# Kernel optimization log

Hardware: AMD Instinct MI355X
Metric: run time of the kernel (lower is better)

## Reference

```python
import jax, jax.numpy as jnp
import numpy as np
import math

H = 128
W = 128
CAM_DIST = 2.0
FOVY = 1.57 / 2.0
SIGMAINV = 7000.0
ERODE = 7
PAD = (ERODE - 1) // 2


def quat_to_rotmat(q):
    # q: [B,4] WXYZ (kornia convention), normalized first
    q = q / jnp.linalg.norm(q, axis=-1, keepdims=True)
    w, x, y, z = q[..., 0], q[..., 1], q[..., 2], q[..., 3]
    R = jnp.stack([
        1 - 2 * (y * y + z * z), 2 * (x * y - w * z), 2 * (x * z + w * y),
        2 * (x * y + w * z), 1 - 2 * (x * x + z * z), 2 * (y * z - w * x),
        2 * (x * z - w * y), 2 * (y * z + w * x), 1 - 2 * (x * x + y * y),
    ], axis=-1)
    return R.reshape(q.shape[:-1] + (3, 3))


def _edge(ax, ay, bx, by, px, py):
    return (px - ax) * (by - ay) - (py - ay) * (bx - ax)


def rasterize(fv_img, fz, fnz, ffeat):
    # fv_img [F,3,2] image-space verts, fz [F,3] camera-space z, fnz [F] normal z, ffeat [F,3,C]
    xs = (jnp.arange(W) + 0.5) / W * 2.0 - 1.0
    ys = 1.0 - (jnp.arange(H) + 0.5) / H * 2.0
    gx, gy = jnp.meshgrid(xs, ys, indexing='xy')   # [H,W]
    PX = gx.reshape(-1, 1)                          # [P,1]
    PY = gy.reshape(-1, 1)
    ax, ay = fv_img[:, 0, 0], fv_img[:, 0, 1]
    bx, by = fv_img[:, 1, 0], fv_img[:, 1, 1]
    cx, cy = fv_img[:, 2, 0], fv_img[:, 2, 1]
    area = _edge(ax, ay, bx, by, cx, cy)            # [F]
    area_s = jnp.where(jnp.abs(area) < 1e-10, 1e-10, area)
    w0 = _edge(bx, by, cx, cy, PX, PY) / area_s     # [P,F] barycentric
    w1 = _edge(cx, cy, ax, ay, PX, PY) / area_s
    w2 = _edge(ax, ay, bx, by, PX, PY) / area_s
    inside = (w0 >= 0) & (w1 >= 0) & (w2 >= 0) & (jnp.abs(area) > 1e-10)
    zpix = w0 * fz[:, 0] + w1 * fz[:, 1] + w2 * fz[:, 2]
    valid = inside & (fnz > 0)                      # back-face cull
    score = jnp.where(valid, zpix, -1e30)           # camera looks down -z: max z is closest
    best = jnp.argmax(score, axis=1)                # [P]
    has = jnp.any(valid, axis=1)
    red = jnp.where(has, best, -1)
    P = PX.shape[0]
    pidx = jnp.arange(P)
    wsel = jnp.stack([w0[pidx, best], w1[pidx, best], w2[pidx, best]], -1)  # [P,3]
    feat = jnp.einsum('pk,pkc->pc', wsel, ffeat[best])
    feat = jnp.where(has[:, None], feat, 0.0)
    # DIB-R soft silhouette: p_f = exp(-d^2*sigmainv) (d=0 inside), A = 1 - prod(1-p_f)
    def seg_d2(a, b):
        abx, aby = b[:, 0] - a[:, 0], b[:, 1] - a[:, 1]
        apx, apy = PX - a[:, 0], PY - a[:, 1]
        t = jnp.clip((apx * abx + apy * aby) / (abx * abx + aby * aby + 1e-12), 0.0, 1.0)
        dx, dy = apx - t * abx, apy - t * aby
        return dx * dx + dy * dy
    d2 = jnp.minimum(jnp.minimum(seg_d2(fv_img[:, 0], fv_img[:, 1]),
                                 seg_d2(fv_img[:, 1], fv_img[:, 2])),
                     seg_d2(fv_img[:, 2], fv_img[:, 0]))
    d2 = jnp.where(inside, 0.0, d2)
    prob = jnp.clip(jnp.exp(-d2 * SIGMAINV), 0.0, 1.0 - 1e-4) * (fnz > 0)
    soft = 1.0 - jnp.exp(jnp.sum(jnp.log1p(-prob), axis=1))
    C = ffeat.shape[-1]
    return feat.reshape(H, W, C), soft.reshape(H, W), red.reshape(H, W)


def bilinear(tex, uv):
    # tex [3,T,T], uv [H,W,2] in [0,1]; torch grid_sample-style bilinear, align_corners=False
    T = tex.shape[-1]
    u = jnp.clip(uv[..., 0], 0.0, 1.0)
    v = jnp.clip(uv[..., 1], 0.0, 1.0)
    x = u * T - 0.5
    y = (1.0 - v) * T - 0.5   # kaolin texture_mapping flips v
    x0 = jnp.floor(x)
    y0 = jnp.floor(y)
    wx = x - x0
    wy = y - y0
    x0i = jnp.clip(x0.astype(jnp.int32), 0, T - 1)
    x1i = jnp.clip(x0i + 1, 0, T - 1)
    y0i = jnp.clip(y0.astype(jnp.int32), 0, T - 1)
    y1i = jnp.clip(y0i + 1, 0, T - 1)
    t00 = tex[:, y0i, x0i]
    t01 = tex[:, y0i, x1i]
    t10 = tex[:, y1i, x0i]
    t11 = tex[:, y1i, x1i]
    return (1 - wy) * ((1 - wx) * t00 + wx * t01) + wy * ((1 - wx) * t10 + wx * t11)


def render_frame(tvec, q, unit_vertices, faces, face_features, texture_maps):
    R = quat_to_rotmat(q)                                        # [B,3,3]
    verts = jnp.einsum('bij,bvj->bvi', R, unit_vertices) + tvec  # rotate about origin + translate
    p_cam = verts - jnp.array([0.0, 0.0, CAM_DIST], dtype=verts.dtype)  # camera at (0,0,d), look-at origin
    ratio = W / H
    tanf = math.tan(FOVY / 2.0)
    negz = -p_cam[..., 2]
    img = jnp.stack([p_cam[..., 0] / (ratio * tanf) / negz,
                     p_cam[..., 1] / tanf / negz], axis=-1)      # [B,V,2]
    fv_img = img[:, faces]                                       # [B,F,3,2]
    fz = p_cam[..., 2][:, faces]                                 # [B,F,3]
    fv_cam = p_cam[:, faces]                                     # [B,F,3,3]
    n = jnp.cross(fv_cam[:, :, 1] - fv_cam[:, :, 0], fv_cam[:, :, 2] - fv_cam[:, :, 0])
    fnz = n[..., 2] / (jnp.linalg.norm(n, axis=-1) + 1e-10)      # [B,F]
    feat, soft, red = jax.vmap(rasterize)(fv_img, fz, fnz, face_features)
    rgb = jax.vmap(bilinear)(texture_maps, feat)                 # [B,3,H,W]
    # erosion with all-ones kernel == grayscale min-pool (borders padded with +inf)
    mask = jax.lax.reduce_window(soft, jnp.inf, jax.lax.min,
                                 (1, ERODE, ERODE), (1, 1, 1),
                                 [(0, 0), (PAD, PAD), (PAD, PAD)])
    Fn = faces.shape[0]
    redw = jnp.where(red < 0, Fn - 1, red)                       # torch -1 index wraps to last face
    depth = jax.vmap(lambda z, r: z[r].mean(-1))(fz, redw)       # [B,H,W]
    return jnp.concatenate([rgb, mask[:, None], depth[:, None]], axis=1)  # [B,5,H,W]


def setup_inputs():
    key = jax.random.key(0)
    ks = jax.random.split(key, 6)
    B, NF, V, F, T = 1, 4, 256, 512, 256
    return {
        'translation': jax.random.uniform(ks[0], (B, 1, NF, 3), minval=-0.3, maxval=0.3),
        'quaternion': jax.random.normal(ks[1], (B, NF, 4)),
        'unit_vertices': jax.random.uniform(ks[2], (B, V, 3), minval=-0.5, maxval=0.5),
        'face_features': jax.random.uniform(ks[3], (B, F, 3, 2)),
        'texture_maps': jax.random.uniform(ks[4], (B, 3, T, T)),
        'faces': jax.random.randint(ks[5], (F, 3), 0, V),
    }


def reference(translation, quaternion, unit_vertices, face_features, texture_maps, faces):
    tseq = jnp.moveaxis(translation, 2, 0)   # [NF,B,1,3]
    qseq = jnp.moveaxis(quaternion, 1, 0)    # [NF,B,4]
    def step(carry, tq):
        t, q = tq
        return carry, render_frame(t, q, unit_vertices, faces, face_features, texture_maps)
    _, outs = jax.lax.scan(step, None, (tseq, qseq))  # [NF,B,5,H,W]
    return jnp.moveaxis(outs, 0, 1)[:, :, None]       # [B,NF,1,5,H,W]
```

## Files before the change

### kernel.cpp

```cpp
#include <hip/hip_runtime.h>
#include <math.h>

#define NFRM 4
#define NFACE 512
#define TT 256
#define REC 32
#define TANF32 0.413980342966f
#define LOG1M_CONST -9.21017456f
#define D2_CUTOFF 0.004286f
#define MARGIN 0.0656f

__device__ __forceinline__ float fm(float a, float b) { return __fmul_rn(a, b); }
__device__ __forceinline__ float fa2(float a, float b) { return __fadd_rn(a, b); }
__device__ __forceinline__ float fs2(float a, float b) { return __fsub_rn(a, b); }
__device__ __forceinline__ float fd2(float a, float b) { return __fdiv_rn(a, b); }


__global__ void setup_kernel(const float* __restrict__ trans,
                             const float* __restrict__ quat,
                             const float* __restrict__ uverts,
                             const int* __restrict__ faces,
                             float* __restrict__ recs,
                             float4* __restrict__ bbox4) {
    int idx = blockIdx.x * blockDim.x + threadIdx.x;
    if (idx >= NFRM * NFACE) return;
    int frame = idx >> 9;
    int face  = idx & (NFACE - 1);

    float qw = quat[frame * 4 + 0];
    float qx = quat[frame * 4 + 1];
    float qy = quat[frame * 4 + 2];
    float qz = quat[frame * 4 + 3];
    float qn = sqrtf(fa2(fa2(fa2(fm(qw, qw), fm(qx, qx)), fm(qy, qy)), fm(qz, qz)));
    qw = fd2(qw, qn); qx = fd2(qx, qn); qy = fd2(qy, qn); qz = fd2(qz, qn);

    float r00 = fs2(1.f, fm(2.f, fa2(fm(qy, qy), fm(qz, qz))));
    float r01 = fm(2.f, fs2(fm(qx, qy), fm(qw, qz)));
    float r02 = fm(2.f, fa2(fm(qx, qz), fm(qw, qy)));
    float r10 = fm(2.f, fa2(fm(qx, qy), fm(qw, qz)));
    float r11 = fs2(1.f, fm(2.f, fa2(fm(qx, qx), fm(qz, qz))));
    float r12 = fm(2.f, fs2(fm(qy, qz), fm(qw, qx)));
    float r20 = fm(2.f, fs2(fm(qx, qz), fm(qw, qy)));
    float r21 = fm(2.f, fa2(fm(qy, qz), fm(qw, qx)));
    float r22 = fs2(1.f, fm(2.f, fa2(fm(qx, qx), fm(qy, qy))));

    float tx = trans[frame * 3 + 0];
    float ty = trans[frame * 3 + 1];
    float tz = trans[frame * 3 + 2];

    float camx[3], camy[3], camz[3], ix[3], iy[3];
    for (int k = 0; k < 3; ++k) {
        int vi = faces[face * 3 + k];
        float ux = uverts[vi * 3 + 0];
        float uy = uverts[vi * 3 + 1];
        float uz = uverts[vi * 3 + 2];
        float X = fa2(fa2(fa2(fm(r00, ux), fm(r01, uy)), fm(r02, uz)), tx);
        float Y = fa2(fa2(fa2(fm(r10, ux), fm(r11, uy)), fm(r12, uz)), ty);
        float Z = fs2(fa2(fa2(fa2(fm(r20, ux), fm(r21, uy)), fm(r22, uz)), tz), 2.0f);
        float negz = -Z;
        camx[k] = X; camy[k] = Y; camz[k] = Z;
        ix[k] = fd2(fd2(X, TANF32), negz);
        iy[k] = fd2(fd2(Y, TANF32), negz);
    }

    float e1cx = fs2(camx[1], camx[0]), e1cy = fs2(camy[1], camy[0]);
    float e2cx = fs2(camx[2], camx[0]), e2cy = fs2(camy[2], camy[0]);
    float nz = fs2(fm(e1cx, e2cy), fm(e1cy, e2cx));

    float ax = ix[0], ay = iy[0], bx = ix[1], by = iy[1], cx = ix[2], cy = iy[2];
    float area = fs2(fm(fs2(cx, ax), fs2(by, ay)), fm(fs2(cy, ay), fs2(bx, ax)));
    bool areaok = fabsf(area) > 1e-10f;
    float area_s = (fabsf(area) < 1e-10f) ? 1e-10f : area;

    float e0x = fs2(cx, bx), e0y = fs2(cy, by);
    float e1x = fs2(ax, cx), e1y = fs2(ay, cy);
    float e2x = fs2(bx, ax), e2y = fs2(by, ay);

    float* r = recs + (size_t)idx * REC;
    r[0] = 0.f; r[1] = 0.f; r[2] = 0.f; r[3] = 0.f;
    r[4] = areaok ? 1.f : 2.f;
    r[5] = (area_s >= 0.f) ? 1.f : -1.f;
    r[6] = fd2(1.0f, area_s);
    r[7] = 0.f;
    r[8]  = ax; r[9]  = ay; r[10] = e2x; r[11] = e2y;
    r[12] = bx; r[13] = by; r[14] = e0x; r[15] = e0y;
    r[16] = cx; r[17] = cy; r[18] = e1x; r[19] = e1y;
    r[20] = camz[0]; r[21] = camz[1]; r[22] = camz[2]; r[23] = 0.f;
    r[24] = fd2(1.0f, fa2(fa2(fm(e2x, e2x), fm(e2y, e2y)), 1e-12f));
    r[25] = fd2(1.0f, fa2(fa2(fm(e0x, e0x), fm(e0y, e0y)), 1e-12f));
    r[26] = fd2(1.0f, fa2(fa2(fm(e1x, e1x), fm(e1y, e1y)), 1e-12f));
    r[27] = 0.f; r[28] = 0.f; r[29] = 0.f; r[30] = 0.f; r[31] = 0.f;

    float4 bb;
    if (nz > 0.f) {
        bb.x = fminf(fminf(ax, bx), cx);
        bb.y = fmaxf(fmaxf(ax, bx), cx);
        bb.z = fminf(fminf(ay, by), cy);
        bb.w = fmaxf(fmaxf(ay, by), cy);
    } else {
        bb.x = 1e30f; bb.y = -1e30f; bb.z = 1e30f; bb.w = -1e30f;
    }
    bbox4[idx] = bb;
}

__global__ __launch_bounds__(256, 4) void raster_kernel(
        const float* __restrict__ recs,
        const float4* __restrict__ bbox4,
        const float* __restrict__ ffeat,
        const float* __restrict__ tex,
        float* __restrict__ out,
        float* __restrict__ softbuf) {
    __shared__ int s_list[NFACE];
    __shared__ int s_cnt[4];
    __shared__ float s_score[256], s_w0[256], s_w1[256], s_w2[256], s_acc[256];
    __shared__ int s_best[256];

    int frame   = blockIdx.x >> 8;
    int tileIdx = blockIdx.x & 255;
    int txo = (tileIdx & 15) * 8;
    int tyo = (tileIdx >> 4) * 8;

    int chunk = threadIdx.x >> 6;
    int lane  = threadIdx.x & 63;
    int w = txo + (lane & 7);
    int h = tyo + (lane >> 3);
    int p = h * 128 + w;
    float px = (w + 0.5f) * (1.0f / 64.0f) - 1.0f;
    float py = 1.0f - (h + 0.5f) * (1.0f / 64.0f);

    float txmin = (txo + 0.5f) * (1.0f / 64.0f) - 1.0f - MARGIN;
    float txmax = (txo + 7.5f) * (1.0f / 64.0f) - 1.0f + MARGIN;
    float tymin = 1.0f - (tyo + 7.5f) * (1.0f / 64.0f) - MARGIN;
    float tymax = 1.0f - (tyo + 0.5f) * (1.0f / 64.0f) + MARGIN;

    const float4* bbF = bbox4 + frame * NFACE;
    unsigned long long m0, m1;
    {
        float4 b0 = bbF[chunk * 128 + lane];
        float4 b1 = bbF[chunk * 128 + 64 + lane];
        bool p0 = (b0.x <= txmax) & (b0.y >= txmin) & (b0.z <= tymax) & (b0.w >= tymin);
        bool p1 = (b1.x <= txmax) & (b1.y >= txmin) & (b1.z <= tymax) & (b1.w >= tymin);
        m0 = __ballot(p0);
        m1 = __ballot(p1);
    }
    if (lane == 0) s_cnt[chunk] = __popcll(m0) + __popcll(m1);
    __syncthreads();
    int base = 0;
    for (int c = 0; c < chunk; ++c) base += s_cnt[c];
    int total = s_cnt[0] + s_cnt[1] + s_cnt[2] + s_cnt[3];
    unsigned long long ltmask = (1ull << lane) - 1ull;
    if ((m0 >> lane) & 1)
        s_list[base + __popcll(m0 & ltmask)] = chunk * 128 + lane;
    if ((m1 >> lane) & 1)
        s_list[base + __popcll(m0) + __popcll(m1 & ltmask)] = chunk * 128 + 64 + lane;
    __syncthreads();

    const float* recF = recs + (size_t)frame * NFACE * REC;
    float bestScore = -1e30f;
    int best = -1;
    float bw0 = 0.f, bw1 = 0.f, bw2 = 0.f;
    float acc = 0.f;

    int lo = (total * chunk) >> 2;
    int hi = (total * (chunk + 1)) >> 2;
    #pragma unroll 2
    for (int i = lo; i < hi; ++i) {
        int f = __builtin_amdgcn_readfirstlane(s_list[i]);
        const float* r = recF + ((size_t)f << 5);
        float flag = r[4];
        float ax = r[8],  ay = r[9],  e2x = r[10], e2y = r[11];
        float bx = r[12], by = r[13], e0x = r[14], e0y = r[15];
        float cx = r[16], cy = r[17], e1x = r[18], e1y = r[19];
        float apx = fs2(px, ax), apy = fs2(py, ay);
        float bpx = fs2(px, bx), bpy = fs2(py, by);
        float cpx = fs2(px, cx), cpy = fs2(py, cy);
        float n0 = fs2(fm(bpx, e0y), fm(bpy, e0x));
        float n1 = fs2(fm(cpx, e1y), fm(cpy, e1x));
        float n2 = fs2(fm(apx, e2y), fm(apy, e2x));
        float sgn = r[5];
        bool inside = (flag == 1.f) & (fm(n0, sgn) >= 0.f)
                    & (fm(n1, sgn) >= 0.f) & (fm(n2, sgn) >= 0.f);
        if (inside) {
            float ia = r[6];
            float w0 = fm(n0, ia), w1v = fm(n1, ia), w2v = fm(n2, ia);
            float zpix = fa2(fa2(fm(w0, r[20]), fm(w1v, r[21])), fm(w2v, r[22]));
            if (zpix > bestScore) {
                bestScore = zpix; best = f; bw0 = w0; bw1 = w1v; bw2 = w2v;
            }
            acc += LOG1M_CONST;
        } else {
            float t0 = fminf(fmaxf((apx * e2x + apy * e2y) * r[24], 0.f), 1.f);
            float dx0 = apx - t0 * e2x, dy0 = apy - t0 * e2y;
            float d2 = dx0 * dx0 + dy0 * dy0;
            float t1 = fminf(fmaxf((bpx * e0x + bpy * e0y) * r[25], 0.f), 1.f);
            float dx1 = bpx - t1 * e0x, dy1 = bpy - t1 * e0y;
            d2 = fminf(d2, dx1 * dx1 + dy1 * dy1);
            float t2 = fminf(fmaxf((cpx * e1x + cpy * e1y) * r[26], 0.f), 1.f);
            float dx2 = cpx - t2 * e1x, dy2 = cpy - t2 * e1y;
            d2 = fminf(d2, dx2 * dx2 + dy2 * dy2);
            if (d2 < D2_CUTOFF) {
                float pr = fminf(__expf(d2 * -7000.f), 0.9999f);
                acc += __logf(1.0f - pr);
            }
        }
    }

    s_score[threadIdx.x] = bestScore;
    s_best[threadIdx.x] = best;
    s_w0[threadIdx.x] = bw0; s_w1[threadIdx.x] = bw1; s_w2[threadIdx.x] = bw2;
    s_acc[threadIdx.x] = acc;
    __syncthreads();

    if (threadIdx.x < 64) {
        int i = threadIdx.x;
        bestScore = s_score[i]; best = s_best[i];
        bw0 = s_w0[i]; bw1 = s_w1[i]; bw2 = s_w2[i];
        acc = s_acc[i];
        for (int c = 1; c < 4; ++c) {
            int j = c * 64 + i;
            float sc = s_score[j];
            if (sc > bestScore) {
                bestScore = sc; best = s_best[j];
                bw0 = s_w0[j]; bw1 = s_w1[j]; bw2 = s_w2[j];
            }
            acc += s_acc[j];
        }
        float fu = 0.f, fv = 0.f;
        if (best >= 0) {
            const float* fb = ffeat + best * 6;
            fu = bw0 * fb[0] + bw1 * fb[2] + bw2 * fb[4];
            fv = bw0 * fb[1] + bw1 * fb[3] + bw2 * fb[5];
        }
        float u = fminf(fmaxf(fu, 0.f), 1.f);
        float v = fminf(fmaxf(fv, 0.f), 1.f);
        float x = u * (float)TT - 0.5f;
        float y = (1.0f - v) * (float)TT - 0.5f;
        float x0f = floorf(x), y0f = floorf(y);
        float wx = x - x0f, wy = y - y0f;
        int x0 = min(max((int)x0f, 0), TT - 1);
        int x1 = min(x0 + 1, TT - 1);
        int y0 = min(max((int)y0f, 0), TT - 1);
        int y1 = min(y0 + 1, TT - 1);
        size_t obase = (size_t)frame * 5 * 16384 + p;
        for (int c = 0; c < 3; ++c) {
            const float* tc = tex + c * (TT * TT);
            float t00 = tc[y0 * TT + x0];
            float t01 = tc[y0 * TT + x1];
            float t10 = tc[y1 * TT + x0];
            float t11 = tc[y1 * TT + x1];
            float rgb = (1.f - wy) * ((1.f - wx) * t00 + wx * t01)
                      + wy * ((1.f - wx) * t10 + wx * t11);
            out[obase + (size_t)c * 16384] = rgb;
        }
        int redw = (best >= 0) ? best : (NFACE - 1);
        const float* rr = recF + ((size_t)redw << 5);
        float depth = fd2(fa2(fa2(rr[20], rr[21]), rr[22]), 3.0f);
        out[obase + 4ull * 16384] = depth;
        float soft = 1.0f - __expf(acc);
        softbuf[frame * 16384 + p] = soft;
    }
}

__global__ void minpool_kernel(const float* __restrict__ softbuf,
                               float* __restrict__ out) {
    int idx = blockIdx.x * 256 + threadIdx.x;
    if (idx >= NFRM * 16384) return;
    int frame = idx >> 14;
    int p = idx & 16383;
    int h = p >> 7, w = p & 127;
    const float* sb = softbuf + frame * 16384;
    float m = INFINITY;
    int h0 = max(h - 3, 0), h1 = min(h + 3, 127);
    int w0 = max(w - 3, 0), w1 = min(w + 3, 127);
    for (int hh = h0; hh <= h1; ++hh)
        for (int ww = w0; ww <= w1; ++ww)
            m = fminf(m, sb[hh * 128 + ww]);
    out[(size_t)frame * 5 * 16384 + 3ull * 16384 + p] = m;
}

extern "C" void kernel_launch(void* const* d_in, const int* in_sizes, int n_in,
                              void* d_out, int out_size, void* d_ws, size_t ws_size,
                              hipStream_t stream) {
    const float* trans  = (const float*)d_in[0];
    const float* quat   = (const float*)d_in[1];
    const float* uverts = (const float*)d_in[2];
    const float* ffeat  = (const float*)d_in[3];
    const float* tex    = (const float*)d_in[4];
    const int*   faces  = (const int*)d_in[5];
    float* out = (float*)d_out;

    float* recs    = (float*)d_ws;
    float4* bbox4  = (float4*)(recs + NFRM * NFACE * REC);
    float* softbuf = (float*)(bbox4 + NFRM * NFACE);

    setup_kernel<<<(NFRM * NFACE + 255) / 256, 256, 0, stream>>>(trans, quat, uverts, faces, recs, bbox4);
    raster_kernel<<<NFRM * 256, 256, 0, stream>>>(recs, bbox4, ffeat, tex, out, softbuf);
    minpool_kernel<<<NFRM * 16384 / 256, 256, 0, stream>>>(softbuf, out);
}
```

Measured before the change: 95.85 us.

## Split faces across two raster blocks per tile and merge in combine kernel

The raster kernel now splits the 512 faces into two halves, launching twice as many blocks, each writing partial depth-test and soft-silhouette results to workspace. A new combine kernel merges the two halves, then does texture sampling, depth and soft-mask output. Tile order is bit-reversed to spread work across CUs, and face indices are loaded once per 64-face batch and broadcast with readlane instead of one LDS read per face. This adds a kernel launch and extra global traffic for the partial buffers in exchange for more parallelism and better load balance. Tie-breaking between halves uses a strict greater-than comparison, so the lower-index face wins ties, which matches argmax.

```diff
diff --git a/kernel.cpp b/kernel.cpp
--- a/kernel.cpp
+++ b/kernel.cpp
@@ -3,6 +3,7 @@
 
 #define NFRM 4
 #define NFACE 512
+#define HALF 256
 #define TT 256
 #define REC 32
 #define TANF32 0.413980342966f
@@ -106,17 +107,19 @@
 __global__ __launch_bounds__(256, 4) void raster_kernel(
         const float* __restrict__ recs,
         const float4* __restrict__ bbox4,
-        const float* __restrict__ ffeat,
-        const float* __restrict__ tex,
-        float* __restrict__ out,
-        float* __restrict__ softbuf) {
-    __shared__ int s_list[NFACE];
+        float* __restrict__ pscore, int* __restrict__ pbest,
+        float* __restrict__ pw0, float* __restrict__ pw1,
+        float* __restrict__ pw2, float* __restrict__ pacc) {
+    __shared__ int s_list[HALF];
     __shared__ int s_cnt[4];
     __shared__ float s_score[256], s_w0[256], s_w1[256], s_w2[256], s_acc[256];
     __shared__ int s_best[256];
 
-    int frame   = blockIdx.x >> 8;
-    int tileIdx = blockIdx.x & 255;
+    int b = blockIdx.x;
+    int tileIdx = (int)(__brev((unsigned)(b & 255)) >> 24);
+    int frame = (b >> 8) & 3;
+    int half  = b >> 10;
+    int fbase = half * HALF;
     int txo = (tileIdx & 15) * 8;
     int tyo = (tileIdx >> 4) * 8;
 
@@ -133,27 +136,20 @@
     float tymin = 1.0f - (tyo + 7.5f) * (1.0f / 64.0f) - MARGIN;
     float tymax = 1.0f - (tyo + 0.5f) * (1.0f / 64.0f) + MARGIN;
 
-    const float4* bbF = bbox4 + frame * NFACE;
-    unsigned long long m0, m1;
     {
-        float4 b0 = bbF[chunk * 128 + lane];
-        float4 b1 = bbF[chunk * 128 + 64 + lane];
-        bool p0 = (b0.x <= txmax) & (b0.y >= txmin) & (b0.z <= tymax) & (b0.w >= tymin);
-        bool p1 = (b1.x <= txmax) & (b1.y >= txmin) & (b1.z <= tymax) & (b1.w >= tymin);
-        m0 = __ballot(p0);
-        m1 = __ballot(p1);
-    }
-    if (lane == 0) s_cnt[chunk] = __popcll(m0) + __popcll(m1);
-    __syncthreads();
-    int base = 0;
-    for (int c = 0; c < chunk; ++c) base += s_cnt[c];
+        int face = fbase + chunk * 64 + lane;
+        float4 bb = bbox4[frame * NFACE + face];
+        bool hit = (bb.x <= txmax) & (bb.y >= txmin) & (bb.z <= tymax) & (bb.w >= tymin);
+        unsigned long long m = __ballot(hit);
+        if (lane == 0) s_cnt[chunk] = __popcll(m);
+        __syncthreads();
+        int base = 0;
+        for (int c = 0; c < chunk; ++c) base += s_cnt[c];
+        unsigned long long ltmask = (1ull << lane) - 1ull;
+        if (hit) s_list[base + __popcll(m & ltmask)] = face;
+        __syncthreads();
+    }
     int total = s_cnt[0] + s_cnt[1] + s_cnt[2] + s_cnt[3];
-    unsigned long long ltmask = (1ull << lane) - 1ull;
-    if ((m0 >> lane) & 1)
-        s_list[base + __popcll(m0 & ltmask)] = chunk * 128 + lane;
-    if ((m1 >> lane) & 1)
-        s_list[base + __popcll(m0) + __popcll(m1 & ltmask)] = chunk * 128 + 64 + lane;
-    __syncthreads();
 
     const float* recF = recs + (size_t)frame * NFACE * REC;
     float bestScore = -1e30f;
@@ -163,44 +159,49 @@
 
     int lo = (total * chunk) >> 2;
     int hi = (total * (chunk + 1)) >> 2;
-    #pragma unroll 2
-    for (int i = lo; i < hi; ++i) {
-        int f = __builtin_amdgcn_readfirstlane(s_list[i]);
-        const float* r = recF + ((size_t)f << 5);
-        float flag = r[4];
-        float ax = r[8],  ay = r[9],  e2x = r[10], e2y = r[11];
-        float bx = r[12], by = r[13], e0x = r[14], e0y = r[15];
-        float cx = r[16], cy = r[17], e1x = r[18], e1y = r[19];
-        float apx = fs2(px, ax), apy = fs2(py, ay);
-        float bpx = fs2(px, bx), bpy = fs2(py, by);
-        float cpx = fs2(px, cx), cpy = fs2(py, cy);
-        float n0 = fs2(fm(bpx, e0y), fm(bpy, e0x));
-        float n1 = fs2(fm(cpx, e1y), fm(cpy, e1x));
-        float n2 = fs2(fm(apx, e2y), fm(apy, e2x));
-        float sgn = r[5];
-        bool inside = (flag == 1.f) & (fm(n0, sgn) >= 0.f)
-                    & (fm(n1, sgn) >= 0.f) & (fm(n2, sgn) >= 0.f);
-        if (inside) {
-            float ia = r[6];
-            float w0 = fm(n0, ia), w1v = fm(n1, ia), w2v = fm(n2, ia);
-            float zpix = fa2(fa2(fm(w0, r[20]), fm(w1v, r[21])), fm(w2v, r[22]));
-            if (zpix > bestScore) {
-                bestScore = zpix; best = f; bw0 = w0; bw1 = w1v; bw2 = w2v;
-            }
-            acc += LOG1M_CONST;
-        } else {
-            float t0 = fminf(fmaxf((apx * e2x + apy * e2y) * r[24], 0.f), 1.f);
-            float dx0 = apx - t0 * e2x, dy0 = apy - t0 * e2y;
-            float d2 = dx0 * dx0 + dy0 * dy0;
-            float t1 = fminf(fmaxf((bpx * e0x + bpy * e0y) * r[25], 0.f), 1.f);
-            float dx1 = bpx - t1 * e0x, dy1 = bpy - t1 * e0y;
-            d2 = fminf(d2, dx1 * dx1 + dy1 * dy1);
-            float t2 = fminf(fmaxf((cpx * e1x + cpy * e1y) * r[26], 0.f), 1.f);
-            float dx2 = cpx - t2 * e1x, dy2 = cpy - t2 * e1y;
-            d2 = fminf(d2, dx2 * dx2 + dy2 * dy2);
-            if (d2 < D2_CUTOFF) {
-                float pr = fminf(__expf(d2 * -7000.f), 0.9999f);
-                acc += __logf(1.0f - pr);
+    for (int base = lo; base < hi; base += 64) {
+        int nb = min(64, hi - base);
+        int li = base + ((lane < nb) ? lane : (nb - 1));
+        int vlist = s_list[li];
+        #pragma unroll 2
+        for (int j = 0; j < nb; ++j) {
+            int f = __builtin_amdgcn_readlane(vlist, j);
+            const float* r = recF + ((size_t)f << 5);
+            float flag = r[4];
+            float ax = r[8],  ay = r[9],  e2x = r[10], e2y = r[11];
+            float bx = r[12], by = r[13], e0x = r[14], e0y = r[15];
+            float cx = r[16], cy = r[17], e1x = r[18], e1y = r[19];
+            float apx = fs2(px, ax), apy = fs2(py, ay);
+            float bpx = fs2(px, bx), bpy = fs2(py, by);
+            float cpx = fs2(px, cx), cpy = fs2(py, cy);
+            float n0 = fs2(fm(bpx, e0y), fm(bpy, e0x));
+            float n1 = fs2(fm(cpx, e1y), fm(cpy, e1x));
+            float n2 = fs2(fm(apx, e2y), fm(apy, e2x));
+            float sgn = r[5];
+            bool inside = (flag == 1.f) & (fm(n0, sgn) >= 0.f)
+                        & (fm(n1, sgn) >= 0.f) & (fm(n2, sgn) >= 0.f);
+            if (inside) {
+                float ia = r[6];
+                float w0 = fm(n0, ia), w1v = fm(n1, ia), w2v = fm(n2, ia);
+                float zpix = fa2(fa2(fm(w0, r[20]), fm(w1v, r[21])), fm(w2v, r[22]));
+                if (zpix > bestScore) {
+                    bestScore = zpix; best = f; bw0 = w0; bw1 = w1v; bw2 = w2v;
+                }
+                acc += LOG1M_CONST;
+            } else {
+                float t0 = fminf(fmaxf((apx * e2x + apy * e2y) * r[24], 0.f), 1.f);
+                float dx0 = apx - t0 * e2x, dy0 = apy - t0 * e2y;
+                float d2 = dx0 * dx0 + dy0 * dy0;
+                float t1 = fminf(fmaxf((bpx * e0x + bpy * e0y) * r[25], 0.f), 1.f);
+                float dx1 = bpx - t1 * e0x, dy1 = bpy - t1 * e0y;
+                d2 = fminf(d2, dx1 * dx1 + dy1 * dy1);
+                float t2 = fminf(fmaxf((cpx * e1x + cpy * e1y) * r[26], 0.f), 1.f);
+                float dx2 = cpx - t2 * e1x, dy2 = cpy - t2 * e1y;
+                d2 = fminf(d2, dx2 * dx2 + dy2 * dy2);
+                if (d2 < D2_CUTOFF) {
+                    float pr = fminf(__expf(d2 * -7000.f), 0.9999f);
+                    acc += __logf(1.0f - pr);
+                }
             }
         }
     }
@@ -225,40 +226,69 @@
             }
             acc += s_acc[j];
         }
-        float fu = 0.f, fv = 0.f;
-        if (best >= 0) {
-            const float* fb = ffeat + best * 6;
-            fu = bw0 * fb[0] + bw1 * fb[2] + bw2 * fb[4];
-            fv = bw0 * fb[1] + bw1 * fb[3] + bw2 * fb[5];
-        }
-        float u = fminf(fmaxf(fu, 0.f), 1.f);
-        float v = fminf(fmaxf(fv, 0.f), 1.f);
-        float x = u * (float)TT - 0.5f;
-        float y = (1.0f - v) * (float)TT - 0.5f;
-        float x0f = floorf(x), y0f = floorf(y);
-        float wx = x - x0f, wy = y - y0f;
-        int x0 = min(max((int)x0f, 0), TT - 1);
-        int x1 = min(x0 + 1, TT - 1);
-        int y0 = min(max((int)y0f, 0), TT - 1);
-        int y1 = min(y0 + 1, TT - 1);
-        size_t obase = (size_t)frame * 5 * 16384 + p;
-        for (int c = 0; c < 3; ++c) {
-            const float* tc = tex + c * (TT * TT);
-            float t00 = tc[y0 * TT + x0];
-            float t01 = tc[y0 * TT + x1];
-            float t10 = tc[y1 * TT + x0];
-            float t11 = tc[y1 * TT + x1];
-            float rgb = (1.f - wy) * ((1.f - wx) * t00 + wx * t01)
-                      + wy * ((1.f - wx) * t10 + wx * t11);
-            out[obase + (size_t)c * 16384] = rgb;
-        }
-        int redw = (best >= 0) ? best : (NFACE - 1);
-        const float* rr = recF + ((size_t)redw << 5);
-        float depth = fd2(fa2(fa2(rr[20], rr[21]), rr[22]), 3.0f);
-        out[obase + 4ull * 16384] = depth;
-        float soft = 1.0f - __expf(acc);
-        softbuf[frame * 16384 + p] = soft;
-    }
+        size_t o = ((size_t)half * NFRM + frame) * 16384 + p;
+        pscore[o] = bestScore; pbest[o] = best;
+        pw0[o] = bw0; pw1[o] = bw1; pw2[o] = bw2; pacc[o] = acc;
+    }
+}
+
+__global__ void combine_kernel(
+        const float* __restrict__ pscore, const int* __restrict__ pbest,
+        const float* __restrict__ pw0, const float* __restrict__ pw1,
+        const float* __restrict__ pw2, const float* __restrict__ pacc,
+        const float* __restrict__ recs,
+        const float* __restrict__ ffeat,
+        const float* __restrict__ tex,
+        float* __restrict__ out,
+        float* __restrict__ softbuf) {
+    int idx = blockIdx.x * 256 + threadIdx.x;
+    if (idx >= NFRM * 16384) return;
+    int frame = idx >> 14;
+    int p = idx & 16383;
+    size_t o0 = (size_t)frame * 16384 + p;
+    size_t o1 = o0 + (size_t)NFRM * 16384;
+
+    float s0 = pscore[o0], s1 = pscore[o1];
+    bool take1 = (s1 > s0);
+    int best   = take1 ? pbest[o1] : pbest[o0];
+    float bw0  = take1 ? pw0[o1] : pw0[o0];
+    float bw1  = take1 ? pw1[o1] : pw1[o0];
+    float bw2  = take1 ? pw2[o1] : pw2[o0];
+    float acc  = pacc[o0] + pacc[o1];
+
+    float fu = 0.f, fv = 0.f;
+    if (best >= 0) {
+        const float* fb = ffeat + best * 6;
+        fu = bw0 * fb[0] + bw1 * fb[2] + bw2 * fb[4];
+        fv = bw0 * fb[1] + bw1 * fb[3] + bw2 * fb[5];
+    }
+    float u = fminf(fmaxf(fu, 0.f), 1.f);
+    float v = fminf(fmaxf(fv, 0.f), 1.f);
+    float x = u * (float)TT - 0.5f;
+    float y = (1.0f - v) * (float)TT - 0.5f;
+    float x0f = floorf(x), y0f = floorf(y);
+    float wx = x - x0f, wy = y - y0f;
+    int x0 = min(max((int)x0f, 0), TT - 1);
+    int x1 = min(x0 + 1, TT - 1);
+    int y0 = min(max((int)y0f, 0), TT - 1);
+    int y1 = min(y0 + 1, TT - 1);
+    size_t obase = (size_t)frame * 5 * 16384 + p;
+    for (int c = 0; c < 3; ++c) {
+        const float* tc = tex + c * (TT * TT);
+        float t00 = tc[y0 * TT + x0];
+        float t01 = tc[y0 * TT + x1];
+        float t10 = tc[y1 * TT + x0];
+        float t11 = tc[y1 * TT + x1];
+        float rgb = (1.f - wy) * ((1.f - wx) * t00 + wx * t01)
+                  + wy * ((1.f - wx) * t10 + wx * t11);
+        out[obase + (size_t)c * 16384] = rgb;
+    }
+    int redw = (best >= 0) ? best : (NFACE - 1);
+    const float* rr = recs + (size_t)frame * NFACE * REC + ((size_t)redw << 5);
+    float depth = fd2(fa2(fa2(rr[20], rr[21]), rr[22]), 3.0f);
+    out[obase + 4ull * 16384] = depth;
+    float soft = 1.0f - __expf(acc);
+    softbuf[(size_t)frame * 16384 + p] = soft;
 }
 
 __global__ void minpool_kernel(const float* __restrict__ softbuf,
@@ -289,11 +319,22 @@
     const int*   faces  = (const int*)d_in[5];
     float* out = (float*)d_out;
 
+    const size_t NPIX = (size_t)NFRM * 16384;
     float* recs    = (float*)d_ws;
     float4* bbox4  = (float4*)(recs + NFRM * NFACE * REC);
-    float* softbuf = (float*)(bbox4 + NFRM * NFACE);
-
-    setup_kernel<<<(NFRM * NFACE + 255) / 256, 256, 0, stream>>>(trans, quat, uverts, faces, recs, bbox4);
-    raster_kernel<<<NFRM * 256, 256, 0, stream>>>(recs, bbox4, ffeat, tex, out, softbuf);
-    minpool_kernel<<<NFRM * 16384 / 256, 256, 0, stream>>>(softbuf, out);
-}
+    float* pscore  = (float*)(bbox4 + NFRM * NFACE);
+    int*   pbest   = (int*)(pscore + 2 * NPIX);
+    float* pw0     = (float*)(pbest + 2 * NPIX);
+    float* pw1     = pw0 + 2 * NPIX;
+    float* pw2     = pw1 + 2 * NPIX;
+    float* pacc    = pw2 + 2 * NPIX;
+    float* softbuf = pacc + 2 * NPIX;
+
+    setup_kernel<<<(NFRM * NFACE + 255) / 256, 256, 0, stream>>>(
+        trans, quat, uverts, faces, recs, bbox4);
+    raster_kernel<<<NFRM * 256 * 2, 256, 0, stream>>>(
+        recs, bbox4, pscore, pbest, pw0, pw1, pw2, pacc);
+    combine_kernel<<<(NFRM * 16384) / 256, 256, 0, stream>>>(
+        pscore, pbest, pw0, pw1, pw2, pacc, recs, ffeat, tex, out, softbuf);
+    minpool_kernel<<<(NFRM * 16384) / 256, 256, 0, stream>>>(softbuf, out);
+}
```

Measured after the change: 96.57 us. No clear change (+0.8%).

## Prefetch next face record, bit-reverse tile order, and pack edge math

Applied to the files above, without the earlier changes.

The per-face loop now loads the next face's record while the current one is evaluated, a software double-buffer meant to hide the scalar load latency. Tile indices are bit-reversed so neighbouring blocks map to spatially scattered tiles, aiming to even out per-workgroup load across CUs. The outside-triangle distance math is written with 2-wide vectors so the compiler can emit packed FP32 ops. Prefetching raises register pressure under the launch bound, and the packed ops may change rounding slightly in the soft-silhouette path.

```diff
diff --git a/kernel.cpp b/kernel.cpp
--- a/kernel.cpp
+++ b/kernel.cpp
@@ -9,6 +9,8 @@
 #define LOG1M_CONST -9.21017456f
 #define D2_CUTOFF 0.004286f
 #define MARGIN 0.0656f
+
+typedef float v2f __attribute__((ext_vector_type(2)));
 
 __device__ __forceinline__ float fm(float a, float b) { return __fmul_rn(a, b); }
 __device__ __forceinline__ float fa2(float a, float b) { return __fadd_rn(a, b); }
@@ -103,6 +105,23 @@
     bbox4[idx] = bb;
 }
 
+struct FRec {
+    float flag, sgn, ia;
+    float ax, ay, e2x, e2y, bx, by, e0x, e0y, cx, cy, e1x, e1y;
+    float z0, z1, z2, iL2, iL0, iL1;
+};
+__device__ __forceinline__ FRec loadRec(const float* __restrict__ recF, int f) {
+    const float* r = recF + ((size_t)f << 5);
+    FRec o;
+    o.flag = r[4];  o.sgn = r[5];  o.ia  = r[6];
+    o.ax = r[8];  o.ay = r[9];  o.e2x = r[10]; o.e2y = r[11];
+    o.bx = r[12]; o.by = r[13]; o.e0x = r[14]; o.e0y = r[15];
+    o.cx = r[16]; o.cy = r[17]; o.e1x = r[18]; o.e1y = r[19];
+    o.z0 = r[20]; o.z1 = r[21]; o.z2 = r[22];
+    o.iL2 = r[24]; o.iL0 = r[25]; o.iL1 = r[26];
+    return o;
+}
+
 __global__ __launch_bounds__(256, 4) void raster_kernel(
         const float* __restrict__ recs,
         const float4* __restrict__ bbox4,
@@ -115,8 +134,9 @@
     __shared__ float s_score[256], s_w0[256], s_w1[256], s_w2[256], s_acc[256];
     __shared__ int s_best[256];
 
-    int frame   = blockIdx.x >> 8;
-    int tileIdx = blockIdx.x & 255;
+    int b = blockIdx.x;
+    int tileIdx = (int)(__brev((unsigned)(b & 255)) >> 24);
+    int frame = b >> 8;
     int txo = (tileIdx & 15) * 8;
     int tyo = (tileIdx >> 4) * 8;
 
@@ -134,26 +154,23 @@
     float tymax = 1.0f - (tyo + 0.5f) * (1.0f / 64.0f) + MARGIN;
 
     const float4* bbF = bbox4 + frame * NFACE;
-    unsigned long long m0, m1;
     {
         float4 b0 = bbF[chunk * 128 + lane];
         float4 b1 = bbF[chunk * 128 + 64 + lane];
         bool p0 = (b0.x <= txmax) & (b0.y >= txmin) & (b0.z <= tymax) & (b0.w >= tymin);
         bool p1 = (b1.x <= txmax) & (b1.y >= txmin) & (b1.z <= tymax) & (b1.w >= tymin);
-        m0 = __ballot(p0);
-        m1 = __ballot(p1);
-    }
-    if (lane == 0) s_cnt[chunk] = __popcll(m0) + __popcll(m1);
-    __syncthreads();
-    int base = 0;
-    for (int c = 0; c < chunk; ++c) base += s_cnt[c];
+        unsigned long long m0 = __ballot(p0);
+        unsigned long long m1 = __ballot(p1);
+        if (lane == 0) s_cnt[chunk] = __popcll(m0) + __popcll(m1);
+        __syncthreads();
+        int base = 0;
+        for (int c = 0; c < chunk; ++c) base += s_cnt[c];
+        unsigned long long ltmask = (1ull << lane) - 1ull;
+        if (p0) s_list[base + __popcll(m0 & ltmask)] = chunk * 128 + lane;
+        if (p1) s_list[base + __popcll(m0) + __popcll(m1 & ltmask)] = chunk * 128 + 64 + lane;
+        __syncthreads();
+    }
     int total = s_cnt[0] + s_cnt[1] + s_cnt[2] + s_cnt[3];
-    unsigned long long ltmask = (1ull << lane) - 1ull;
-    if ((m0 >> lane) & 1)
-        s_list[base + __popcll(m0 & ltmask)] = chunk * 128 + lane;
-    if ((m1 >> lane) & 1)
-        s_list[base + __popcll(m0) + __popcll(m1 & ltmask)] = chunk * 128 + 64 + lane;
-    __syncthreads();
 
     const float* recF = recs + (size_t)frame * NFACE * REC;
     float bestScore = -1e30f;
@@ -163,45 +180,51 @@
 
     int lo = (total * chunk) >> 2;
     int hi = (total * (chunk + 1)) >> 2;
-    #pragma unroll 2
-    for (int i = lo; i < hi; ++i) {
-        int f = __builtin_amdgcn_readfirstlane(s_list[i]);
-        const float* r = recF + ((size_t)f << 5);
-        float flag = r[4];
-        float ax = r[8],  ay = r[9],  e2x = r[10], e2y = r[11];
-        float bx = r[12], by = r[13], e0x = r[14], e0y = r[15];
-        float cx = r[16], cy = r[17], e1x = r[18], e1y = r[19];
-        float apx = fs2(px, ax), apy = fs2(py, ay);
-        float bpx = fs2(px, bx), bpy = fs2(py, by);
-        float cpx = fs2(px, cx), cpy = fs2(py, cy);
-        float n0 = fs2(fm(bpx, e0y), fm(bpy, e0x));
-        float n1 = fs2(fm(cpx, e1y), fm(cpy, e1x));
-        float n2 = fs2(fm(apx, e2y), fm(apy, e2x));
-        float sgn = r[5];
-        bool inside = (flag == 1.f) & (fm(n0, sgn) >= 0.f)
-                    & (fm(n1, sgn) >= 0.f) & (fm(n2, sgn) >= 0.f);
-        if (inside) {
-            float ia = r[6];
-            float w0 = fm(n0, ia), w1v = fm(n1, ia), w2v = fm(n2, ia);
-            float zpix = fa2(fa2(fm(w0, r[20]), fm(w1v, r[21])), fm(w2v, r[22]));
-            if (zpix > bestScore) {
-                bestScore = zpix; best = f; bw0 = w0; bw1 = w1v; bw2 = w2v;
+    if (lo < hi) {
+        int f_cur = __builtin_amdgcn_readfirstlane(s_list[lo]);
+        FRec cur = loadRec(recF, f_cur);
+        for (int i = lo; i < hi; ++i) {
+            int nj = (i + 1 < hi) ? (i + 1) : i;
+            int f_nxt = __builtin_amdgcn_readfirstlane(s_list[nj]);
+            FRec nxt = loadRec(recF, f_nxt);
+
+            float apx = fs2(px, cur.ax), apy = fs2(py, cur.ay);
+            float bpx = fs2(px, cur.bx), bpy = fs2(py, cur.by);
+            float cpx = fs2(px, cur.cx), cpy = fs2(py, cur.cy);
+            float n0 = fs2(fm(bpx, cur.e0y), fm(bpy, cur.e0x));
+            float n1 = fs2(fm(cpx, cur.e1y), fm(cpy, cur.e1x));
+            float n2 = fs2(fm(apx, cur.e2y), fm(apy, cur.e2x));
+            float sgn = cur.sgn;
+            bool inside = (cur.flag == 1.f) & (fm(n0, sgn) >= 0.f)
+                        & (fm(n1, sgn) >= 0.f) & (fm(n2, sgn) >= 0.f);
+            if (inside) {
+                float ia = cur.ia;
+                float w0 = fm(n0, ia), w1v = fm(n1, ia), w2v = fm(n2, ia);
+                float zpix = fa2(fa2(fm(w0, cur.z0), fm(w1v, cur.z1)), fm(w2v, cur.z2));
+                if (zpix > bestScore) {
+                    bestScore = zpix; best = f_cur; bw0 = w0; bw1 = w1v; bw2 = w2v;
+                }
+                acc += LOG1M_CONST;
+            } else {
+                v2f ap = {apx, apy}, bp = {bpx, bpy}, cp = {cpx, cpy};
+                v2f e2 = {cur.e2x, cur.e2y};
+                v2f e0 = {cur.e0x, cur.e0y};
+                v2f e1 = {cur.e1x, cur.e1y};
+                v2f pa = ap * e2, pb = bp * e0, pc = cp * e1;
+                float t0 = fminf(fmaxf((pa.x + pa.y) * cur.iL2, 0.f), 1.f);
+                float t1 = fminf(fmaxf((pb.x + pb.y) * cur.iL0, 0.f), 1.f);
+                float t2 = fminf(fmaxf((pc.x + pc.y) * cur.iL1, 0.f), 1.f);
+                v2f d0 = ap - t0 * e2;
+                v2f d1 = bp - t1 * e0;
+                v2f d2v = cp - t2 * e1;
+                v2f q0 = d0 * d0, q1 = d1 * d1, q2 = d2v * d2v;
+                float d2 = fminf(fminf(q0.x + q0.y, q1.x + q1.y), q2.x + q2.y);
+                if (d2 < D2_CUTOFF) {
+                    float pr = fminf(__expf(d2 * -7000.f), 0.9999f);
+                    acc += __logf(1.0f - pr);
+                }
             }
-            acc += LOG1M_CONST;
-        } else {
-            float t0 = fminf(fmaxf((apx * e2x + apy * e2y) * r[24], 0.f), 1.f);
-            float dx0 = apx - t0 * e2x, dy0 = apy - t0 * e2y;
-            float d2 = dx0 * dx0 + dy0 * dy0;
-            float t1 = fminf(fmaxf((bpx * e0x + bpy * e0y) * r[25], 0.f), 1.f);
-            float dx1 = bpx - t1 * e0x, dy1 = bpy - t1 * e0y;
-            d2 = fminf(d2, dx1 * dx1 + dy1 * dy1);
-            float t2 = fminf(fmaxf((cpx * e1x + cpy * e1y) * r[26], 0.f), 1.f);
-            float dx2 = cpx - t2 * e1x, dy2 = cpy - t2 * e1y;
-            d2 = fminf(d2, dx2 * dx2 + dy2 * dy2);
-            if (d2 < D2_CUTOFF) {
-                float pr = fminf(__expf(d2 * -7000.f), 0.9999f);
-                acc += __logf(1.0f - pr);
-            }
+            cur = nxt; f_cur = f_nxt;
         }
     }
 
@@ -293,7 +316,9 @@
     float4* bbox4  = (float4*)(recs + NFRM * NFACE * REC);
     float* softbuf = (float*)(bbox4 + NFRM * NFACE);
 
-    setup_kernel<<<(NFRM * NFACE + 255) / 256, 256, 0, stream>>>(trans, quat, uverts, faces, recs, bbox4);
-    raster_kernel<<<NFRM * 256, 256, 0, stream>>>(recs, bbox4, ffeat, tex, out, softbuf);
-    minpool_kernel<<<NFRM * 16384 / 256, 256, 0, stream>>>(softbuf, out);
-}
+    setup_kernel<<<(NFRM * NFACE + 255) / 256, 256, 0, stream>>>(
+        trans, quat, uverts, faces, recs, bbox4);
+    raster_kernel<<<NFRM * 256, 256, 0, stream>>>(
+        recs, bbox4, ffeat, tex, out, softbuf);
+    minpool_kernel<<<(NFRM * 16384) / 256, 256, 0, stream>>>(softbuf, out);
+}
```

Result: no change. 97.15 us (+1.4%).

## Add per-tile edge-distance culling pass and bit-reverse tile ordering

Applied to the files above, without the earlier changes.

Adds a second culling stage after the bounding-box test. For each surviving face it evaluates each edge function at the tile corner most favourable to that edge, and rejects the face when the squared distance to the edge exceeds the soft-silhouette margin. This shrinks the per-pixel face loop, at the cost of an extra compaction pass with two more block barriers per round and a second shared list. Tile indices are also bit-reversed so heavy and light tiles spread across CUs, and the unroll pragma on the main loop is removed.

```diff
diff --git a/kernel.cpp b/kernel.cpp
--- a/kernel.cpp
+++ b/kernel.cpp
@@ -9,6 +9,7 @@
 #define LOG1M_CONST -9.21017456f
 #define D2_CUTOFF 0.004286f
 #define MARGIN 0.0656f
+#define MARGIN2 0.00430336f
 
 __device__ __forceinline__ float fm(float a, float b) { return __fmul_rn(a, b); }
 __device__ __forceinline__ float fa2(float a, float b) { return __fadd_rn(a, b); }
@@ -110,13 +111,15 @@
         const float* __restrict__ tex,
         float* __restrict__ out,
         float* __restrict__ softbuf) {
-    __shared__ int s_list[NFACE];
+    __shared__ int s_listA[NFACE];
+    __shared__ int s_listB[NFACE];
     __shared__ int s_cnt[4];
     __shared__ float s_score[256], s_w0[256], s_w1[256], s_w2[256], s_acc[256];
     __shared__ int s_best[256];
 
-    int frame   = blockIdx.x >> 8;
-    int tileIdx = blockIdx.x & 255;
+    int b = blockIdx.x;
+    int tileIdx = (int)(__brev((unsigned)(b & 255)) >> 24);
+    int frame = b >> 8;
     int txo = (tileIdx & 15) * 8;
     int tyo = (tileIdx >> 4) * 8;
 
@@ -128,44 +131,81 @@
     float px = (w + 0.5f) * (1.0f / 64.0f) - 1.0f;
     float py = 1.0f - (h + 0.5f) * (1.0f / 64.0f);
 
-    float txmin = (txo + 0.5f) * (1.0f / 64.0f) - 1.0f - MARGIN;
-    float txmax = (txo + 7.5f) * (1.0f / 64.0f) - 1.0f + MARGIN;
-    float tymin = 1.0f - (tyo + 7.5f) * (1.0f / 64.0f) - MARGIN;
-    float tymax = 1.0f - (tyo + 0.5f) * (1.0f / 64.0f) + MARGIN;
-
-    const float4* bbF = bbox4 + frame * NFACE;
-    unsigned long long m0, m1;
+    float X0 = (txo + 0.5f) * (1.0f / 64.0f) - 1.0f;
+    float X1 = (txo + 7.5f) * (1.0f / 64.0f) - 1.0f;
+    float Y0 = 1.0f - (tyo + 7.5f) * (1.0f / 64.0f);
+    float Y1 = 1.0f - (tyo + 0.5f) * (1.0f / 64.0f);
+    float txmin = X0 - MARGIN, txmax = X1 + MARGIN;
+    float tymin = Y0 - MARGIN, tymax = Y1 + MARGIN;
+
+    const float* recF = recs + (size_t)frame * NFACE * REC;
+    unsigned long long ltmask = (1ull << lane) - 1ull;
+
+    int totalA;
     {
+        const float4* bbF = bbox4 + frame * NFACE;
         float4 b0 = bbF[chunk * 128 + lane];
         float4 b1 = bbF[chunk * 128 + 64 + lane];
         bool p0 = (b0.x <= txmax) & (b0.y >= txmin) & (b0.z <= tymax) & (b0.w >= tymin);
         bool p1 = (b1.x <= txmax) & (b1.y >= txmin) & (b1.z <= tymax) & (b1.w >= tymin);
-        m0 = __ballot(p0);
-        m1 = __ballot(p1);
-    }
-    if (lane == 0) s_cnt[chunk] = __popcll(m0) + __popcll(m1);
-    __syncthreads();
-    int base = 0;
-    for (int c = 0; c < chunk; ++c) base += s_cnt[c];
-    int total = s_cnt[0] + s_cnt[1] + s_cnt[2] + s_cnt[3];
-    unsigned long long ltmask = (1ull << lane) - 1ull;
-    if ((m0 >> lane) & 1)
-        s_list[base + __popcll(m0 & ltmask)] = chunk * 128 + lane;
-    if ((m1 >> lane) & 1)
-        s_list[base + __popcll(m0) + __popcll(m1 & ltmask)] = chunk * 128 + 64 + lane;
-    __syncthreads();
-
-    const float* recF = recs + (size_t)frame * NFACE * REC;
+        unsigned long long m0 = __ballot(p0);
+        unsigned long long m1 = __ballot(p1);
+        if (lane == 0) s_cnt[chunk] = __popcll(m0) + __popcll(m1);
+        __syncthreads();
+        int base = 0;
+        for (int c = 0; c < chunk; ++c) base += s_cnt[c];
+        totalA = s_cnt[0] + s_cnt[1] + s_cnt[2] + s_cnt[3];
+        if (p0) s_listA[base + __popcll(m0 & ltmask)] = chunk * 128 + lane;
+        if (p1) s_listA[base + __popcll(m0) + __popcll(m1 & ltmask)] = chunk * 128 + 64 + lane;
+        __syncthreads();
+    }
+
+    int totalB = 0;
+    for (int base = 0; base < totalA; base += 256) {
+        int i = base + threadIdx.x;
+        bool keep = false; int f = 0;
+        if (i < totalA) {
+            f = s_listA[i];
+            const float* r = recF + ((size_t)f << 5);
+            float sgn = r[5];
+            float ax = r[8],  ay = r[9],  e2x = r[10], e2y = r[11];
+            float bx = r[12], by = r[13], e0x = r[14], e0y = r[15];
+            float cx = r[16], cy = r[17], e1x = r[18], e1y = r[19];
+            float iL2 = r[24], iL0 = r[25], iL1 = r[26];
+            float q0x = (fm(e0y, sgn) > 0.f) ? X1 : X0;
+            float q0y = (fm(e0x, sgn) > 0.f) ? Y0 : Y1;
+            float g0 = fm(fs2(fm(fs2(q0x, bx), e0y), fm(fs2(q0y, by), e0x)), sgn);
+            bool rej0 = (g0 < 0.f) & (fm(fm(g0, g0), iL0) > MARGIN2);
+            float q1x = (fm(e1y, sgn) > 0.f) ? X1 : X0;
+            float q1y = (fm(e1x, sgn) > 0.f) ? Y0 : Y1;
+            float g1 = fm(fs2(fm(fs2(q1x, cx), e1y), fm(fs2(q1y, cy), e1x)), sgn);
+            bool rej1 = (g1 < 0.f) & (fm(fm(g1, g1), iL1) > MARGIN2);
+            float q2x = (fm(e2y, sgn) > 0.f) ? X1 : X0;
+            float q2y = (fm(e2x, sgn) > 0.f) ? Y0 : Y1;
+            float g2 = fm(fs2(fm(fs2(q2x, ax), e2y), fm(fs2(q2y, ay), e2x)), sgn);
+            bool rej2 = (g2 < 0.f) & (fm(fm(g2, g2), iL2) > MARGIN2);
+            keep = !(rej0 | rej1 | rej2);
+        }
+        unsigned long long m = __ballot(keep);
+        if (lane == 0) s_cnt[chunk] = __popcll(m);
+        __syncthreads();
+        int b2 = totalB;
+        for (int c = 0; c < chunk; ++c) b2 += s_cnt[c];
+        int roundTotal = s_cnt[0] + s_cnt[1] + s_cnt[2] + s_cnt[3];
+        if (keep) s_listB[b2 + __popcll(m & ltmask)] = f;
+        totalB += roundTotal;
+        __syncthreads();
+    }
+
     float bestScore = -1e30f;
     int best = -1;
     float bw0 = 0.f, bw1 = 0.f, bw2 = 0.f;
     float acc = 0.f;
 
-    int lo = (total * chunk) >> 2;
-    int hi = (total * (chunk + 1)) >> 2;
-    #pragma unroll 2
+    int lo = (totalB * chunk) >> 2;
+    int hi = (totalB * (chunk + 1)) >> 2;
     for (int i = lo; i < hi; ++i) {
-        int f = __builtin_amdgcn_readfirstlane(s_list[i]);
+        int f = __builtin_amdgcn_readfirstlane(s_listB[i]);
         const float* r = recF + ((size_t)f << 5);
         float flag = r[4];
         float ax = r[8],  ay = r[9],  e2x = r[10], e2y = r[11];
@@ -293,7 +333,9 @@
     float4* bbox4  = (float4*)(recs + NFRM * NFACE * REC);
     float* softbuf = (float*)(bbox4 + NFRM * NFACE);
 
-    setup_kernel<<<(NFRM * NFACE + 255) / 256, 256, 0, stream>>>(trans, quat, uverts, faces, recs, bbox4);
-    raster_kernel<<<NFRM * 256, 256, 0, stream>>>(recs, bbox4, ffeat, tex, out, softbuf);
-    minpool_kernel<<<NFRM * 16384 / 256, 256, 0, stream>>>(softbuf, out);
+    setup_kernel<<<(NFRM * NFACE + 255) / 256, 256, 0, stream>>>(
+        trans, quat, uverts, faces, recs, bbox4);
+    raster_kernel<<<NFRM * 256, 256, 0, stream>>>(
+        recs, bbox4, ffeat, tex, out, softbuf);
+    minpool_kernel<<<(NFRM * 16384) / 256, 256, 0, stream>>>(softbuf, out);
 }
```

Result: no change. 94.01 us (-1.9%).
